# Kernel optimization log

Measured on AMD Instinct MI355X. Metric: run time of the kernel, lower is better.

Reference implementation:

```python
import jax, jax.numpy as jnp
import numpy as np

N_NODES = 100000
N_EDGES = 600000
NUM_GRAPHS = 512
IN_DIM = 128
HID = 64
HEADS = 2
NEG_SLOPE = 0.2


def gat_layer(h_in, src, dst, W, a_s, a_d, b, n_nodes):
    # W: [F_in, H*C], a_s/a_d: [H, C], b: [H*C]
    H, C = a_s.shape
    h = (h_in @ W).reshape(n_nodes, H, C)            # [N,H,C]
    alpha_src = jnp.einsum('nhc,hc->nh', h, a_s)      # [N,H]
    alpha_dst = jnp.einsum('nhc,hc->nh', h, a_d)      # [N,H]
    e = alpha_src[src] + alpha_dst[dst]               # [E,H]
    e = jnp.where(e >= 0, e, NEG_SLOPE * e)           # leaky_relu
    # segment softmax over destination node
    m = jax.ops.segment_max(e, dst, num_segments=n_nodes)
    m = jnp.where(jnp.isfinite(m), m, 0.0)
    ex = jnp.exp(e - m[dst])                          # [E,H]
    denom = jax.ops.segment_sum(ex, dst, num_segments=n_nodes)
    alpha = ex / jnp.maximum(denom[dst], 1e-16)       # [E,H]
    out = jax.ops.segment_sum(alpha[:, :, None] * h[src], dst, num_segments=n_nodes)
    return out.reshape(n_nodes, H * C) + b


def setup_inputs() -> dict:
    key = jax.random.key(0)
    ks = jax.random.split(key, 16)
    x = jax.random.normal(ks[0], (N_NODES, IN_DIM), dtype=jnp.float32)
    edge_index = jax.random.randint(ks[1], (2, N_EDGES), 0, N_NODES, dtype=jnp.int32)
    batch = jnp.sort(jax.random.randint(ks[2], (N_NODES,), 0, NUM_GRAPHS, dtype=jnp.int32))
    s = lambda *d: 1.0 / np.sqrt(d[0])
    W1 = jax.random.normal(ks[3], (IN_DIM, HEADS * HID), jnp.float32) * s(IN_DIM)
    a_src1 = jax.random.normal(ks[4], (HEADS, HID), jnp.float32) * s(HID)
    a_dst1 = jax.random.normal(ks[5], (HEADS, HID), jnp.float32) * s(HID)
    b1 = jnp.zeros((HEADS * HID,), jnp.float32)
    W2 = jax.random.normal(ks[6], (HEADS * HID, HID), jnp.float32) * s(HEADS * HID)
    a_src2 = jax.random.normal(ks[7], (1, HID), jnp.float32) * s(HID)
    a_dst2 = jax.random.normal(ks[8], (1, HID), jnp.float32) * s(HID)
    b2 = jnp.zeros((HID,), jnp.float32)
    Wf1 = jax.random.normal(ks[9], (2 * HID, HID), jnp.float32) * s(2 * HID)
    bf1 = jnp.zeros((HID,), jnp.float32)
    Wf2 = jax.random.normal(ks[10], (HID, 1), jnp.float32) * s(HID)
    bf2 = jnp.zeros((1,), jnp.float32)
    return dict(x=x, edge_index=edge_index, batch=batch, W1=W1, a_src1=a_src1,
                a_dst1=a_dst1, b1=b1, W2=W2, a_src2=a_src2, a_dst2=a_dst2, b2=b2,
                Wf1=Wf1, bf1=bf1, Wf2=Wf2, bf2=bf2)


def reference(x, edge_index, batch, W1, a_src1, a_dst1, b1, W2, a_src2, a_dst2, b2,
              Wf1, bf1, Wf2, bf2):
    n = x.shape[0]
    loops = jnp.arange(n, dtype=edge_index.dtype)
    src = jnp.concatenate([edge_index[0], loops])
    dst = jnp.concatenate([edge_index[1], loops])
    h = gat_layer(x, src, dst, W1, a_src1, a_dst1, b1, n)
    h = jax.nn.relu(h)
    h = gat_layer(h, src, dst, W2, a_src2, a_dst2, b2, n)  # [N, HID]
    # global mean + max pool per graph
    ones = jnp.ones((n,), h.dtype)
    counts = jax.ops.segment_sum(ones, batch, num_segments=NUM_GRAPHS)  # [G]
    mean = jax.ops.segment_sum(h, batch, num_segments=NUM_GRAPHS) / jnp.maximum(counts, 1.0)[:, None]
    mx = jax.ops.segment_max(h, batch, num_segments=NUM_GRAPHS)
    mx = jnp.where(counts[:, None] > 0, mx, 0.0)
    pooled = jnp.concatenate([mean, mx], axis=1)  # [G, 2*HID]
    out = jax.nn.relu(pooled @ Wf1 + bf1) @ Wf2 + bf2  # [G, 1]
    return out
```

## Files before the change

kernel.cpp:

```cpp
#include <hip/hip_runtime.h>

#define N_NODESC 100000
#define N_EDGESC 600000
#define E_TOTC   700000
#define NUM_GRAPHSC 512
#define NEG_SLOPE 0.2f
#define NEG_INF_ENC 0x007FFFFFu
#define SCAN_NB 128

typedef unsigned short ushort_t;
typedef __attribute__((ext_vector_type(8))) short bf16x8;
typedef __attribute__((ext_vector_type(4))) float f32x4;

__device__ __forceinline__ unsigned enc_f32(float f) {
    unsigned u = __float_as_uint(f);
    return (u & 0x80000000u) ? ~u : (u | 0x80000000u);
}
__device__ __forceinline__ float dec_f32(unsigned u) {
    u = (u & 0x80000000u) ? (u ^ 0x80000000u) : ~u;
    return __uint_as_float(u);
}
__device__ __forceinline__ ushort_t f32_to_bf16(float f) {
    unsigned u = __float_as_uint(f);
    return (ushort_t)((u + 0x7FFFu + ((u >> 16) & 1u)) >> 16);
}
__device__ __forceinline__ float bf16_to_f32(ushort_t h) {
    return __uint_as_float(((unsigned)h) << 16);
}
__device__ __forceinline__ unsigned pack_bf16x2(float a, float b) {
    return (unsigned)f32_to_bf16(a) | ((unsigned)f32_to_bf16(b) << 16);
}

__device__ __forceinline__ void glds16(const void* g, void* l) {
    __builtin_amdgcn_global_load_lds(
        (const __attribute__((address_space(1))) void*)g,
        (__attribute__((address_space(3))) void*)l, 16, 0, 0);
}

__global__ __launch_bounds__(256) void init_all(float* __restrict__ msum,
                                                unsigned* __restrict__ mmax,
                                                float* __restrict__ cnt,
                                                int* __restrict__ deg,
                                                const float* __restrict__ W1,
                                                const float* __restrict__ W2,
                                                ushort_t* __restrict__ wPre1,
                                                ushort_t* __restrict__ wPre2) {
    int i = blockIdx.x * 256 + threadIdx.x;
    if (i < NUM_GRAPHSC * 64) { msum[i] = 0.f; mmax[i] = NEG_INF_ENC; }
    if (i < NUM_GRAPHSC) cnt[i] = 0.f;
    if (i < N_NODESC) deg[i] = 0;
    if (i < 128 * 128) {
        int n = i >> 7, k = i & 127;
        wPre1[n * 128 + k] = f32_to_bf16(W1[k * 128 + n]);
    } else if (i < 128 * 128 + 64 * 128) {
        int j = i - 128 * 128;
        int n = j >> 7, k = j & 127;
        wPre2[n * 128 + k] = f32_to_bf16(W2[k * 64 + n]);
    }
}

__global__ __launch_bounds__(256) void hist_dst(const int* __restrict__ ei,
                                                int* __restrict__ deg) {
    int e = blockIdx.x * blockDim.x + threadIdx.x;
    if (e >= E_TOTC) return;
    int d = (e < N_EDGESC) ? ei[N_EDGESC + e] : e - N_EDGESC;
    atomicAdd(&deg[d], 1);
}

__global__ __launch_bounds__(256) void scan_partial(const int* __restrict__ deg,
                                                    int* __restrict__ bsum, int n) {
    __shared__ int red[256];
    int chunk = (n + SCAN_NB - 1) / SCAN_NB;
    int lo = blockIdx.x * chunk, hi = min(lo + chunk, n);
    int s = 0;
    for (int i = lo + threadIdx.x; i < hi; i += 256) s += deg[i];
    red[threadIdx.x] = s;
    __syncthreads();
    for (int d = 128; d; d >>= 1) {
        if (threadIdx.x < d) red[threadIdx.x] += red[threadIdx.x + d];
        __syncthreads();
    }
    if (threadIdx.x == 0) bsum[blockIdx.x] = red[0];
}

__global__ __launch_bounds__(256) void scan_final(const int* __restrict__ deg,
                                                  const int* __restrict__ bsum,
                                                  int* __restrict__ off, int n) {
    __shared__ int bs[SCAN_NB];
    __shared__ int tile[256];
    __shared__ int carry;
    int t = threadIdx.x;
    if (t < SCAN_NB) bs[t] = bsum[t];
    __syncthreads();
    for (int d = 1; d < SCAN_NB; d <<= 1) {
        int v = (t >= d && t < SCAN_NB) ? bs[t - d] : 0;
        __syncthreads();
        if (t < SCAN_NB) bs[t] += v;
        __syncthreads();
    }
    if (t == 0) carry = blockIdx.x ? bs[blockIdx.x - 1] : 0;
    __syncthreads();
    int chunk = (n + SCAN_NB - 1) / SCAN_NB;
    int lo = blockIdx.x * chunk, hi = min(lo + chunk, n);
    for (int base = lo; base < hi; base += 256) {
        int i = base + t;
        int v = (i < hi) ? deg[i] : 0;
        tile[t] = v;
        __syncthreads();
        for (int d = 1; d < 256; d <<= 1) {
            int u = (t >= d) ? tile[t - d] : 0;
            __syncthreads();
            tile[t] += u;
            __syncthreads();
        }
        if (i < hi) off[i] = carry + tile[t] - v;
        __syncthreads();
        if (t == 0) carry += tile[255];
        __syncthreads();
    }
}

__global__ __launch_bounds__(256) void scatter_csr(const int* __restrict__ ei,
                                                   int* __restrict__ off,
                                                   int* __restrict__ csr) {
    int e = blockIdx.x * blockDim.x + threadIdx.x;
    if (e >= E_TOTC) return;
    int s, d;
    if (e < N_EDGESC) { s = ei[e]; d = ei[N_EDGESC + e]; } else { s = d = e - N_EDGESC; }
    int slot = atomicAdd(&off[d], 1);
    csr[slot] = s;
}

__global__ __launch_bounds__(64) void gemm1_mfma(const float* __restrict__ X,
                                                 const ushort_t* __restrict__ Wp,
                                                 const float* __restrict__ a_s,
                                                 const float* __restrict__ a_d,
                                                 float* __restrict__ as_out,
                                                 float* __restrict__ ad_out,
                                                 ushort_t* __restrict__ Y16, int N) {
    __shared__ float sx[2048];
    int lane = threadIdx.x;
    int quad = lane >> 4, l16 = lane & 15;
    size_t node0 = (size_t)blockIdx.x * 16;

    {
        int rhalf = lane >> 5;
        int cb = (lane & 31) * 16;
#pragma unroll
        for (int c = 0; c < 8; ++c) {
            int rl = 2 * c + rhalf;
            size_t grow = node0 + rl;
            if (grow >= (size_t)N) grow = N - 1;
            int goff = cb ^ ((rl & 15) << 4);
            glds16((const char*)(X + grow * 128) + goff,
                   (char*)sx + c * 1024);
        }
    }
    asm volatile("s_waitcnt vmcnt(0)" ::: "memory");
    __builtin_amdgcn_sched_barrier(0);

    const char* swx = (const char*)sx + l16 * 512;
    int skey = (l16 & 15) << 4;

    f32x4 acc[8];
#pragma unroll
    for (int ct = 0; ct < 8; ++ct) acc[ct] = (f32x4){0.f, 0.f, 0.f, 0.f};

#pragma unroll
    for (int kc = 0; kc < 4; ++kc) {
        int b = kc * 128 + quad * 32;
        float4 xa = *(const float4*)(swx + (b ^ skey));
        float4 xb = *(const float4*)(swx + ((b + 16) ^ skey));
        union { bf16x8 v; unsigned u[4]; } af;
        af.u[0] = pack_bf16x2(xa.x, xa.y);
        af.u[1] = pack_bf16x2(xa.z, xa.w);
        af.u[2] = pack_bf16x2(xb.x, xb.y);
        af.u[3] = pack_bf16x2(xb.z, xb.w);
#pragma unroll
        for (int ct = 0; ct < 8; ++ct) {
            bf16x8 bb = *(const bf16x8*)(Wp + (size_t)(ct * 16 + l16) * 128 + kc * 32 + quad * 8);
            acc[ct] = __builtin_amdgcn_mfma_f32_16x16x32_bf16(af.v, bb, acc[ct], 0, 0, 0);
        }
    }

    unsigned* Yu = (unsigned*)Y16;
    float asv0[4], asv1[4], adv0[4], adv1[4];
#pragma unroll
    for (int ct = 0; ct < 4; ++ct) {
        int c = ct * 16 + l16;
        asv0[ct] = a_s[c]; asv1[ct] = a_s[64 + c];
        adv0[ct] = a_d[c]; adv1[ct] = a_d[64 + c];
    }
#pragma unroll
    for (int r = 0; r < 4; ++r) {
        size_t row = node0 + quad * 4 + r;
        bool ok = row < (size_t)N;
        if (ok) {
#pragma unroll
            for (int ct = 0; ct < 4; ++ct)
                Yu[row * 64 + ct * 16 + l16] = pack_bf16x2(acc[ct][r], acc[ct + 4][r]);
        }
        float ps0 = 0.f, pd0 = 0.f, ps1 = 0.f, pd1 = 0.f;
#pragma unroll
        for (int ct = 0; ct < 4; ++ct) {
            ps0 += acc[ct][r] * asv0[ct];     pd0 += acc[ct][r] * adv0[ct];
            ps1 += acc[ct + 4][r] * asv1[ct]; pd1 += acc[ct + 4][r] * adv1[ct];
        }
#pragma unroll
        for (int sh = 1; sh < 16; sh <<= 1) {
            ps0 += __shfl_xor(ps0, sh); pd0 += __shfl_xor(pd0, sh);
            ps1 += __shfl_xor(ps1, sh); pd1 += __shfl_xor(pd1, sh);
        }
        if (l16 == 0 && ok) {
            *(float2*)(as_out + row * 2) = make_float2(ps0, ps1);
            *(float2*)(ad_out + row * 2) = make_float2(pd0, pd1);
        }
    }
}

template <int H, bool RELU, bool FUSE2, bool FPOOL>
__global__ __launch_bounds__(256) void gat_gather(const int* __restrict__ off_end,
                                                  const int* __restrict__ deg,
                                                  const int* __restrict__ csr,
                                                  const float* __restrict__ as,
                                                  const float* __restrict__ ad,
                                                  const ushort_t* __restrict__ H16,
                                                  const float* __restrict__ b,
                                                  void* __restrict__ outp,
                                                  const ushort_t* __restrict__ Wp2,
                                                  const float* __restrict__ as2v,
                                                  const float* __restrict__ ad2v,
                                                  float* __restrict__ as2o,
                                                  float* __restrict__ ad2o,
                                                  ushort_t* __restrict__ h2out,
                                                  const int* __restrict__ batchp,
                                                  float* __restrict__ msum,
                                                  unsigned* __restrict__ mmax,
                                                  float* __restrict__ cntb,
                                                  int N) {
    __shared__ char h1tile[16 * 256];
    __shared__ float aspart[16][4];
    __shared__ float adpart[16][4];
    __shared__ int batch_l[16];
    int lane = threadIdx.x & 63;
    int wave = threadIdx.x >> 6;
    int l = lane & 15;
    int gbase = lane & 48;
    int n = blockIdx.x * 16 + wave * 4 + (lane >> 4);
    if (n >= N) return;
    int dg = deg[n];
    int o = off_end[n] - dg;
    float adv[H];
#pragma unroll
    for (int h = 0; h < H; ++h) adv[h] = ad[n * H + h];

    float acc[H][4], den[H];
#pragma unroll
    for (int h = 0; h < H; ++h) {
        den[h] = 0.f;
#pragma unroll
        for (int q = 0; q < 4; ++q) acc[h][q] = 0.f;
    }

    const unsigned* Hu = (const unsigned*)H16;

    for (int base = 0; base < dg; base += 16) {
        int i = base + l;
        bool valid = i < dg;
        int s = valid ? csr[o + i] : 0;
        float v[H];
        if (H == 2) {
            float2 p = valid ? ((const float2*)as)[s] : make_float2(0.f, 0.f);
            v[0] = p.x + adv[0];
            v[H - 1] = p.y + adv[H - 1];
        } else {
            v[0] = valid ? as[s] + adv[0] : 0.f;
        }
#pragma unroll
        for (int h = 0; h < H; ++h) {
            float e = v[h] >= 0.f ? v[h] : NEG_SLOPE * v[h];
            v[h] = valid ? __expf(e) : 0.f;
            den[h] += v[h];
        }
        int wpk = (H == 2) ? (int)pack_bf16x2(v[0], v[H - 1])
                           : (int)__float_as_uint(v[0]);
        int cnt = min(dg - base, 16);
        int cnt4 = (cnt + 3) & ~3;
        for (int j = 0; j < cnt4; j += 4) {
#pragma unroll
            for (int u = 0; u < 4; ++u) {
                int src = gbase + j + u;
                int sj = __shfl(s, src);
                int wp = __shfl(wpk, src);
                if (H == 2) {
                    float w0 = __uint_as_float(((unsigned)wp) << 16);
                    float w1 = __uint_as_float(((unsigned)wp) & 0xffff0000u);
                    uint4 hu = *(const uint4*)(Hu + (size_t)sj * 64 + l * 4);
                    acc[0][0] += w0 * __uint_as_float(hu.x << 16);
                    acc[H - 1][0] += w1 * __uint_as_float(hu.x & 0xffff0000u);
                    acc[0][1] += w0 * __uint_as_float(hu.y << 16);
                    acc[H - 1][1] += w1 * __uint_as_float(hu.y & 0xffff0000u);
                    acc[0][2] += w0 * __uint_as_float(hu.z << 16);
                    acc[H - 1][2] += w1 * __uint_as_float(hu.z & 0xffff0000u);
                    acc[0][3] += w0 * __uint_as_float(hu.w << 16);
                    acc[H - 1][3] += w1 * __uint_as_float(hu.w & 0xffff0000u);
                } else {
                    float w0 = __uint_as_float((unsigned)wp);
                    uint2 hu = *(const uint2*)((const unsigned*)(H16 + (size_t)sj * 64) + l * 2);
                    acc[0][0] += w0 * __uint_as_float(hu.x << 16);
                    acc[0][1] += w0 * __uint_as_float(hu.x & 0xffff0000u);
                    acc[0][2] += w0 * __uint_as_float(hu.y << 16);
                    acc[0][3] += w0 * __uint_as_float(hu.y & 0xffff0000u);
                }
            }
        }
    }
#pragma unroll
    for (int h = 0; h < H; ++h) {
#pragma unroll
        for (int sh = 8; sh; sh >>= 1) den[h] += __shfl_xor(den[h], sh);
    }
    if (H == 2) {
        float4 b0 = *(const float4*)(b + l * 4);
        float4 b1 = *(const float4*)(b + 64 + l * 4);
        float r0[4], r1[4];
        float id0 = 1.f / fmaxf(den[0], 1e-16f);
        float id1 = 1.f / fmaxf(den[H - 1], 1e-16f);
        r0[0] = acc[0][0] * id0 + b0.x; r0[1] = acc[0][1] * id0 + b0.y;
        r0[2] = acc[0][2] * id0 + b0.z; r0[3] = acc[0][3] * id0 + b0.w;
        r1[0] = acc[H - 1][0] * id1 + b1.x; r1[1] = acc[H - 1][1] * id1 + b1.y;
        r1[2] = acc[H - 1][2] * id1 + b1.z; r1[3] = acc[H - 1][3] * id1 + b1.w;
        if (RELU) {
#pragma unroll
            for (int q = 0; q < 4; ++q) { r0[q] = fmaxf(r0[q], 0.f); r1[q] = fmaxf(r1[q], 0.f); }
        }
        uint2 p0 = make_uint2(pack_bf16x2(r0[0], r0[1]), pack_bf16x2(r0[2], r0[3]));
        uint2 p1 = make_uint2(pack_bf16x2(r1[0], r1[1]), pack_bf16x2(r1[2], r1[3]));
        if (FUSE2) {
            int g = threadIdx.x >> 4;
            int key = (g & 15) << 4;
            *(uint2*)(h1tile + g * 256 + ((l * 8) ^ key)) = p0;
            *(uint2*)(h1tile + g * 256 + ((128 + l * 8) ^ key)) = p1;
        } else {
            ushort_t* outb = (ushort_t*)outp;
            *(uint2*)(outb + (size_t)n * 128 + l * 4) = p0;
            *(uint2*)(outb + (size_t)n * 128 + 64 + l * 4) = p1;
        }
    } else {
        float4 bv = *(const float4*)(b + l * 4);
        float id0 = 1.f / fmaxf(den[0], 1e-16f);
        float4 r;
        r.x = acc[0][0] * id0 + bv.x; r.y = acc[0][1] * id0 + bv.y;
        r.z = acc[0][2] * id0 + bv.z; r.w = acc[0][3] * id0 + bv.w;
        if (RELU) { r.x = fmaxf(r.x, 0.f); r.y = fmaxf(r.y, 0.f);
                    r.z = fmaxf(r.z, 0.f); r.w = fmaxf(r.w, 0.f); }
        if (FPOOL) {
            float* pt = (float*)h1tile;
            int gl = threadIdx.x >> 4;
            *(float4*)(pt + gl * 64 + l * 4) = r;
        } else {
            *(float4*)((float*)outp + (size_t)n * 64 + l * 4) = r;
        }
    }

    if (FPOOL) {
        if (threadIdx.x < 16) batch_l[threadIdx.x] = batchp[blockIdx.x * 16 + threadIdx.x];
        __syncthreads();
        if (threadIdx.x < 64) {
            int c = threadIdx.x;
            const float* pt = (const float*)h1tile;
            int curg = batch_l[0];
            float s = 0.f, m = -1e30f;
            int cc = 0;
#pragma unroll
            for (int i = 0; i < 16; ++i) {
                int gg = batch_l[i];
                float v = pt[i * 64 + c];
                if (gg != curg) {
                    atomicAdd(&msum[curg * 64 + c], s);
                    atomicMax(&mmax[curg * 64 + c], enc_f32(m));
                    if (c == 0) atomicAdd(&cntb[curg], (float)cc);
                    s = 0.f; m = -1e30f; cc = 0; curg = gg;
                }
                s += v;
                m = fmaxf(m, v);
                ++cc;
            }
            atomicAdd(&msum[curg * 64 + c], s);
            atomicMax(&mmax[curg * 64 + c], enc_f32(m));
            if (c == 0) atomicAdd(&cntb[curg], (float)cc);
        }
    }

    if (FUSE2) {
        __syncthreads();
        int quad = lane >> 4, l16 = lane & 15;
        int skey = (l16 & 15) << 4;
        const char* swx = h1tile + l16 * 256;
        f32x4 acc2 = (f32x4){0.f, 0.f, 0.f, 0.f};
#pragma unroll
        for (int kc = 0; kc < 4; ++kc) {
            int bb_ = kc * 64 + quad * 16;
            bf16x8 a = *(const bf16x8*)(swx + (bb_ ^ skey));
            bf16x8 bb = *(const bf16x8*)(Wp2 + (size_t)(wave * 16 + l16) * 128 + kc * 32 + quad * 8);
            acc2 = __builtin_amdgcn_mfma_f32_16x16x32_bf16(a, bb, acc2, 0, 0, 0);
        }
        float asv = as2v[wave * 16 + l16], adv2 = ad2v[wave * 16 + l16];
        size_t node0 = (size_t)blockIdx.x * 16;
#pragma unroll
        for (int r = 0; r < 4; ++r) {
            size_t row = node0 + quad * 4 + r;
            h2out[row * 64 + wave * 16 + l16] = f32_to_bf16(acc2[r]);
            float ps = acc2[r] * asv, pd = acc2[r] * adv2;
#pragma unroll
            for (int sh = 1; sh < 16; sh <<= 1) {
                ps += __shfl_xor(ps, sh);
                pd += __shfl_xor(pd, sh);
            }
            if (l16 == 0) {
                aspart[quad * 4 + r][wave] = ps;
                adpart[quad * 4 + r][wave] = pd;
            }
        }
        __syncthreads();
        int t = threadIdx.x;
        if (t < 16) {
            as2o[node0 + t] = aspart[t][0] + aspart[t][1] + aspart[t][2] + aspart[t][3];
        } else if (t < 32) {
            int rr = t - 16;
            ad2o[node0 + rr] = adpart[rr][0] + adpart[rr][1] + adpart[rr][2] + adpart[rr][3];
        }
    }
}

__global__ __launch_bounds__(64) void mlp_head(const float* __restrict__ msum,
                                               const unsigned* __restrict__ mmax,
                                               const float* __restrict__ cnt,
                                               const float* __restrict__ Wf1,
                                               const float* __restrict__ bf1,
                                               const float* __restrict__ Wf2,
                                               const float* __restrict__ bf2,
                                               float* __restrict__ out) {
    __shared__ float pooled[128];
    int g = blockIdx.x, lane = threadIdx.x;
    float c = cnt[g];
    pooled[lane] = msum[g * 64 + lane] / fmaxf(c, 1.0f);
    pooled[64 + lane] = (c > 0.f) ? dec_f32(mmax[g * 64 + lane]) : 0.f;
    __syncthreads();
    float acc = bf1[lane];
#pragma unroll
    for (int k = 0; k < 128; ++k) acc += pooled[k] * Wf1[k * 64 + lane];
    acc = fmaxf(acc, 0.f);
    float r = acc * Wf2[lane];
#pragma unroll
    for (int off = 32; off; off >>= 1) r += __shfl_xor(r, off);
    if (lane == 0) out[g] = r + bf2[0];
}

extern "C" void kernel_launch(void* const* d_in, const int* in_sizes, int n_in,
                              void* d_out, int out_size, void* d_ws, size_t ws_size,
                              hipStream_t stream) {
    const float* x    = (const float*)d_in[0];
    const int*   ei   = (const int*)d_in[1];
    const int*   batch= (const int*)d_in[2];
    const float* W1   = (const float*)d_in[3];
    const float* as1  = (const float*)d_in[4];
    const float* ad1  = (const float*)d_in[5];
    const float* b1   = (const float*)d_in[6];
    const float* W2   = (const float*)d_in[7];
    const float* as2  = (const float*)d_in[8];
    const float* ad2  = (const float*)d_in[9];
    const float* b2   = (const float*)d_in[10];
    const float* Wf1  = (const float*)d_in[11];
    const float* bf1  = (const float*)d_in[12];
    const float* Wf2  = (const float*)d_in[13];
    const float* bf2  = (const float*)d_in[14];
    float* out = (float*)d_out;

    const size_t N = N_NODESC;
    float* ws = (float*)d_ws;
    ushort_t* h16_1 = (ushort_t*)ws;
    ushort_t* out1b = (ushort_t*)(ws + N * 64);
    ushort_t* h16_2 = (ushort_t*)(ws + N * 128);
    float*    out2  = ws + N * 160;
    float*    small = ws + N * 224;
    float*    as1b = small;
    float*    ad1b = small + 2 * N;
    float*    as2b = small + 4 * N;
    float*    ad2b = small + 5 * N;
    float*    msum = small + 6 * N;
    unsigned* mmax = (unsigned*)(small + 6 * N + 512 * 64);
    float*    cntb = small + 6 * N + 2 * 512 * 64;
    int* ip  = (int*)(small + 6 * N + 2 * 512 * 64 + 512);
    int* deg  = ip;
    int* off  = ip + N;
    int* csr  = ip + 2 * N;
    int* bsum = ip + 2 * N + E_TOTC;
    ushort_t* wPre1 = (ushort_t*)(bsum + SCAN_NB);
    ushort_t* wPre2 = wPre1 + 128 * 128;
    (void)out1b; (void)out2;

    init_all<<<(N_NODESC + 255) / 256, 256, 0, stream>>>(msum, mmax, cntb, deg,
                                                         W1, W2, wPre1, wPre2);

    hist_dst<<<(E_TOTC + 255) / 256, 256, 0, stream>>>(ei, deg);
    scan_partial<<<SCAN_NB, 256, 0, stream>>>(deg, bsum, N);
    scan_final<<<SCAN_NB, 256, 0, stream>>>(deg, bsum, off, N);
    scatter_csr<<<(E_TOTC + 255) / 256, 256, 0, stream>>>(ei, off, csr);

    const int NBLK16 = (N_NODESC + 15) / 16;

    gemm1_mfma<<<NBLK16, 64, 0, stream>>>(x, wPre1, as1, ad1, as1b, ad1b, h16_1, N);
    gat_gather<2, true, true, false><<<NBLK16, 256, 0, stream>>>(
        off, deg, csr, as1b, ad1b, h16_1, b1, nullptr,
        wPre2, as2, ad2, as2b, ad2b, h16_2,
        nullptr, nullptr, nullptr, nullptr, N);

    gat_gather<1, false, false, true><<<NBLK16, 256, 0, stream>>>(
        off, deg, csr, as2b, ad2b, h16_2, b2, nullptr,
        nullptr, nullptr, nullptr, nullptr, nullptr, nullptr,
        batch, msum, mmax, cntb, N);

    mlp_head<<<NUM_GRAPHSC, 64, 0, stream>>>(msum, mmax, cntb, Wf1, bf1, Wf2, bf2, out);
}
```

Baseline: 285.9 us.

## Pre-convert X to bf16 in init and fuse degree histogram into gemm1

```diff
diff --git a/kernel.cpp b/kernel.cpp
--- a/kernel.cpp
+++ b/kernel.cpp
@@ -44,7 +44,9 @@
                                                 const float* __restrict__ W1,
                                                 const float* __restrict__ W2,
                                                 ushort_t* __restrict__ wPre1,
-                                                ushort_t* __restrict__ wPre2) {
+                                                ushort_t* __restrict__ wPre2,
+                                                const float* __restrict__ X,
+                                                ushort_t* __restrict__ xb16) {
     int i = blockIdx.x * 256 + threadIdx.x;
     if (i < NUM_GRAPHSC * 64) { msum[i] = 0.f; mmax[i] = NEG_INF_ENC; }
     if (i < NUM_GRAPHSC) cnt[i] = 0.f;
@@ -57,14 +59,16 @@
         int n = j >> 7, k = j & 127;
         wPre2[n * 128 + k] = f32_to_bf16(W2[k * 64 + n]);
     }
-}
-
-__global__ __launch_bounds__(256) void hist_dst(const int* __restrict__ ei,
-                                                int* __restrict__ deg) {
-    int e = blockIdx.x * blockDim.x + threadIdx.x;
-    if (e >= E_TOTC) return;
-    int d = (e < N_EDGESC) ? ei[N_EDGESC + e] : e - N_EDGESC;
-    atomicAdd(&deg[d], 1);
+    if (i < N_NODESC * 128 / 8) {
+        const float4* xp = (const float4*)(X + (size_t)i * 8);
+        float4 a = xp[0], b = xp[1];
+        uint4 o;
+        o.x = pack_bf16x2(a.x, a.y);
+        o.y = pack_bf16x2(a.z, a.w);
+        o.z = pack_bf16x2(b.x, b.y);
+        o.w = pack_bf16x2(b.z, b.w);
+        *(uint4*)(xb16 + (size_t)i * 8) = o;
+    }
 }
 
 __global__ __launch_bounds__(256) void scan_partial(const int* __restrict__ deg,
@@ -131,35 +135,41 @@
     csr[slot] = s;
 }
 
-__global__ __launch_bounds__(64) void gemm1_mfma(const float* __restrict__ X,
+__global__ __launch_bounds__(64) void gemm1_mfma(const ushort_t* __restrict__ Xb,
                                                  const ushort_t* __restrict__ Wp,
                                                  const float* __restrict__ a_s,
                                                  const float* __restrict__ a_d,
                                                  float* __restrict__ as_out,
                                                  float* __restrict__ ad_out,
-                                                 ushort_t* __restrict__ Y16, int N) {
-    __shared__ float sx[2048];
+                                                 ushort_t* __restrict__ Y16,
+                                                 const int* __restrict__ ei,
+                                                 int* __restrict__ deg, int N) {
+    __shared__ ushort_t sx[2048];
     int lane = threadIdx.x;
     int quad = lane >> 4, l16 = lane & 15;
     size_t node0 = (size_t)blockIdx.x * 16;
 
     {
-        int rhalf = lane >> 5;
-        int cb = (lane & 31) * 16;
-#pragma unroll
-        for (int c = 0; c < 8; ++c) {
-            int rl = 2 * c + rhalf;
+        int rq = lane >> 4;
+        int cb = (lane & 15) * 16;
+#pragma unroll
+        for (int c = 0; c < 4; ++c) {
+            int rl = 4 * c + rq;
             size_t grow = node0 + rl;
             if (grow >= (size_t)N) grow = N - 1;
             int goff = cb ^ ((rl & 15) << 4);
-            glds16((const char*)(X + grow * 128) + goff,
+            glds16((const char*)(Xb + grow * 128) + goff,
                    (char*)sx + c * 1024);
         }
+    }
+    for (int e = blockIdx.x * 64 + lane; e < E_TOTC; e += 6250 * 64) {
+        int d = (e < N_EDGESC) ? ei[N_EDGESC + e] : e - N_EDGESC;
+        atomicAdd(&deg[d], 1);
     }
     asm volatile("s_waitcnt vmcnt(0)" ::: "memory");
     __builtin_amdgcn_sched_barrier(0);
 
-    const char* swx = (const char*)sx + l16 * 512;
+    const char* swx = (const char*)sx + l16 * 256;
     int skey = (l16 & 15) << 4;
 
     f32x4 acc[8];
@@ -168,18 +178,12 @@
 
 #pragma unroll
     for (int kc = 0; kc < 4; ++kc) {
-        int b = kc * 128 + quad * 32;
-        float4 xa = *(const float4*)(swx + (b ^ skey));
-        float4 xb = *(const float4*)(swx + ((b + 16) ^ skey));
-        union { bf16x8 v; unsigned u[4]; } af;
-        af.u[0] = pack_bf16x2(xa.x, xa.y);
-        af.u[1] = pack_bf16x2(xa.z, xa.w);
-        af.u[2] = pack_bf16x2(xb.x, xb.y);
-        af.u[3] = pack_bf16x2(xb.z, xb.w);
+        int b = kc * 64 + quad * 16;
+        bf16x8 a = *(const bf16x8*)(swx + (b ^ skey));
 #pragma unroll
         for (int ct = 0; ct < 8; ++ct) {
             bf16x8 bb = *(const bf16x8*)(Wp + (size_t)(ct * 16 + l16) * 128 + kc * 32 + quad * 8);
-            acc[ct] = __builtin_amdgcn_mfma_f32_16x16x32_bf16(af.v, bb, acc[ct], 0, 0, 0);
+            acc[ct] = __builtin_amdgcn_mfma_f32_16x16x32_bf16(a, bb, acc[ct], 0, 0, 0);
         }
     }
 
@@ -480,9 +484,8 @@
     const size_t N = N_NODESC;
     float* ws = (float*)d_ws;
     ushort_t* h16_1 = (ushort_t*)ws;
-    ushort_t* out1b = (ushort_t*)(ws + N * 64);
+    ushort_t* xb16  = (ushort_t*)(ws + N * 64);
     ushort_t* h16_2 = (ushort_t*)(ws + N * 128);
-    float*    out2  = ws + N * 160;
     float*    small = ws + N * 224;
     float*    as1b = small;
     float*    ad1b = small + 2 * N;
@@ -498,19 +501,20 @@
     int* bsum = ip + 2 * N + E_TOTC;
     ushort_t* wPre1 = (ushort_t*)(bsum + SCAN_NB);
     ushort_t* wPre2 = wPre1 + 128 * 128;
-    (void)out1b; (void)out2;
-
-    init_all<<<(N_NODESC + 255) / 256, 256, 0, stream>>>(msum, mmax, cntb, deg,
-                                                         W1, W2, wPre1, wPre2);
-
-    hist_dst<<<(E_TOTC + 255) / 256, 256, 0, stream>>>(ei, deg);
+
+    const int NBLK16 = (N_NODESC + 15) / 16;
+    const int NBLKI  = (N_NODESC * 128 / 8 + 255) / 256;
+
+    init_all<<<NBLKI, 256, 0, stream>>>(msum, mmax, cntb, deg, W1, W2,
+                                        wPre1, wPre2, x, xb16);
+
+    gemm1_mfma<<<NBLK16, 64, 0, stream>>>(xb16, wPre1, as1, ad1, as1b, ad1b,
+                                          h16_1, ei, deg, N);
+
     scan_partial<<<SCAN_NB, 256, 0, stream>>>(deg, bsum, N);
     scan_final<<<SCAN_NB, 256, 0, stream>>>(deg, bsum, off, N);
     scatter_csr<<<(E_TOTC + 255) / 256, 256, 0, stream>>>(ei, off, csr);
 
-    const int NBLK16 = (N_NODESC + 15) / 16;
-
-    gemm1_mfma<<<NBLK16, 64, 0, stream>>>(x, wPre1, as1, ad1, as1b, ad1b, h16_1, N);
     gat_gather<2, true, true, false><<<NBLK16, 256, 0, stream>>>(
         off, deg, csr, as1b, ad1b, h16_1, b1, nullptr,
         wPre2, as2, ad2, as2b, ad2b, h16_2,
```

After: 290.3 us. About the same (+1.5%).
